# Kernel optimization log

Hardware: AMD Instinct MI355X
Metric: run time of the kernel (lower is better)

The kernel has to match this reference:

```python
import jax, jax.numpy as jnp
import numpy as np

NUM_HEADS = 16

def setup_inputs() -> dict:
    key = jax.random.key(0)
    k_x, k_wq, k_bq, k_wo, k_bo = jax.random.split(key, 5)
    B, S, D = 4, 2048, 1024
    x = jax.random.normal(k_x, (B, S, D), dtype=jnp.float32)
    # Flax Dense default init: lecun_normal for kernel, zeros for bias; use small normals here.
    w_qkv = jax.random.normal(k_wq, (D, 3 * D), dtype=jnp.float32) * (D ** -0.5)
    b_qkv = jnp.zeros((3 * D,), dtype=jnp.float32)
    w_out = jax.random.normal(k_wo, (D, D), dtype=jnp.float32) * (D ** -0.5)
    b_out = jnp.zeros((D,), dtype=jnp.float32)
    return {"x": x, "w_qkv": w_qkv, "b_qkv": b_qkv, "w_out": w_out, "b_out": b_out}

def reference(x, w_qkv, b_qkv, w_out, b_out):
    B, S, D = x.shape
    H = NUM_HEADS
    hd = D // H
    scale = hd ** -0.5
    qkv = x @ w_qkv + b_qkv                                  # [B,S,3D]
    qkv = qkv.reshape(B, S, 3, H, hd)
    qkv = jnp.transpose(qkv, (2, 0, 3, 1, 4))                # [3,B,H,S,hd]
    q, k, v = qkv[0], qkv[1], qkv[2]
    attn = jnp.einsum("bhqd,bhkd->bhqk", q, k) * scale       # [B,H,S,S]
    attn = jax.nn.softmax(attn, axis=-1)
    out = jnp.einsum("bhqk,bhkd->bhqd", attn, v)             # [B,H,S,hd]
    out = jnp.transpose(out, (0, 2, 1, 3)).reshape(B, S, D)
    return out @ w_out + b_out
```

## Files before the change

### kernel.cpp

```cpp
#include <hip/hip_runtime.h>
#include <cstdint>
#include <cstddef>

#define B_    4
#define S_    2048
#define D_    1024
#define H_    16
#define HD_   64
#define M_    8192
#define NQKV  3072

typedef __bf16 bf16;
typedef __bf16 bf16x4 __attribute__((ext_vector_type(4)));
typedef __bf16 bf16x8 __attribute__((ext_vector_type(8)));
typedef float  f32x2  __attribute__((ext_vector_type(2)));
typedef float  f32x4  __attribute__((ext_vector_type(4)));
typedef float  f32x16 __attribute__((ext_vector_type(16)));
typedef uint32_t u32x2 __attribute__((ext_vector_type(2)));
typedef uint32_t u32x4 __attribute__((ext_vector_type(4)));

#define MFMA16(a, b, c) __builtin_amdgcn_mfma_f32_16x16x32_bf16(a, b, c, 0, 0, 0)

__device__ __forceinline__ void gl2lds16(const void* g, void* l) {
  __builtin_amdgcn_global_load_lds(
      (__attribute__((address_space(1))) void*)(uintptr_t)g,
      (__attribute__((address_space(3))) void*)l, 16, 0, 0);
}

__device__ __forceinline__ uint32_t pkbf16(float a, float b) {
  union { bf16 h[2]; uint32_t u; } z;
  z.h[0] = (bf16)a; z.h[1] = (bf16)b;
  return z.u;
}

__global__ __launch_bounds__(256) void cast_f32_bf16(const float* __restrict__ in,
                                                     bf16* __restrict__ out, int n4) {
  int i = blockIdx.x * 256 + threadIdx.x;
  if (i >= n4) return;
  float4 v = ((const float4*)in)[i];
  bf16x4 o;
  o[0] = (bf16)v.x; o[1] = (bf16)v.y; o[2] = (bf16)v.z; o[3] = (bf16)v.w;
  ((bf16x4*)out)[i] = o;
}

__global__ __launch_bounds__(256) void transpose_cast(const float* __restrict__ in,
                                                      bf16* __restrict__ out, int R, int C) {
  __shared__ float tile[32][33];
  int bx = blockIdx.x * 32, by = blockIdx.y * 32;
  int tx = threadIdx.x, ty = threadIdx.y;
#pragma unroll
  for (int i = 0; i < 32; i += 8)
    tile[ty + i][tx] = in[(size_t)(by + ty + i) * C + bx + tx];
  __syncthreads();
#pragma unroll
  for (int i = 0; i < 32; i += 8)
    out[(size_t)(bx + ty + i) * R + by + tx] = (bf16)tile[tx][ty + i];
}

template <bool OUT_BF16>
__global__ __launch_bounds__(512, 2) void gemm256(const bf16* __restrict__ A,
                                                  const bf16* __restrict__ Bt,
                                                  const float* __restrict__ bias,
                                                  void* __restrict__ Cptr,
                                                  int M, int N, int K) {
  extern __shared__ __align__(16) bf16 sm[];
  const int tid  = threadIdx.x;
  const int lane = tid & 63, w = tid >> 6;
  const int lo   = lane & 15, quad = lane >> 4;
  const int wr   = w >> 1, wc = w & 1;
  const int xcd  = blockIdx.x & 7, g = blockIdx.x >> 3;
  const int mi_  = g & 3, n_ = g >> 2;
  const int bm   = (xcd * 4 + mi_) * 256, bn = n_ * 128;

  const bf16* Ag = A  + (size_t)bm * K;
  const bf16* Bg = Bt + (size_t)bn * K;

  const int swzl  = lo & 7;
  const int laneA = (wr * 64 + lo) * 64;
  const int laneB = (wc * 64 + lo) * 64;
  const int pc0   = (quad ^ swzl) * 8;
  const int pc1   = ((4 + quad) ^ swzl) * 8;

  int aoffG[4], boffG[2];
#pragma unroll
  for (int la = 0; la < 4; ++la) {
    int ca = la * 512 + tid, row = ca >> 3, s = ca & 7;
    aoffG[la] = row * K + ((s ^ (row & 7)) * 8);
  }
#pragma unroll
  for (int lb = 0; lb < 2; ++lb) {
    int cb = lb * 512 + tid, row = cb >> 3, s = cb & 7;
    boffG[lb] = row * K + ((s ^ (row & 7)) * 8);
  }
  const int T = K >> 6;

  f32x4 acc[4][4];
  const f32x4 zero = {0.f, 0.f, 0.f, 0.f};
#pragma unroll
  for (int i = 0; i < 4; ++i)
#pragma unroll
    for (int j = 0; j < 4; ++j) acc[i][j] = zero;

#pragma unroll
  for (int la = 0; la < 4; ++la)
    gl2lds16(Ag + aoffG[la], sm + (la * 512 + tid) * 8);
#pragma unroll
  for (int lb = 0; lb < 2; ++lb)
    gl2lds16(Bg + boffG[lb], sm + 16384 + (lb * 512 + tid) * 8);
#pragma unroll
  for (int la = 0; la < 4; ++la)
    gl2lds16(Ag + 64 + aoffG[la], sm + 24576 + (la * 512 + tid) * 8);
#pragma unroll
  for (int lb = 0; lb < 2; ++lb)
    gl2lds16(Bg + 64 + boffG[lb], sm + 24576 + 16384 + (lb * 512 + tid) * 8);
  asm volatile("s_waitcnt vmcnt(6)" ::: "memory");
  __builtin_amdgcn_s_barrier();

  auto body = [&](int t, bool st) __attribute__((always_inline)) {
    bf16* As_ = sm + (t % 3) * 24576;
    bf16* Bs_ = As_ + 16384;
    bf16* An_ = sm + ((t + 2) % 3) * 24576;
    bf16* Bn_ = An_ + 16384;
    const size_t kg = (size_t)(t + 2) * 64;
    bf16x8 av0, av1, bv[4];

    av0 = *(const bf16x8*)&As_[laneA + 0 * 1024 + pc0];
    av1 = *(const bf16x8*)&As_[laneA + 1 * 1024 + pc0];
#pragma unroll
    for (int j = 0; j < 4; ++j)
      bv[j] = *(const bf16x8*)&Bs_[laneB + j * 1024 + pc0];
    if (st) {
      gl2lds16(Ag + kg + aoffG[0], An_ + (0 * 512 + tid) * 8);
      gl2lds16(Ag + kg + aoffG[1], An_ + (1 * 512 + tid) * 8);
    }
    __builtin_amdgcn_s_barrier();
    __builtin_amdgcn_s_setprio(1);
#pragma unroll
    for (int j = 0; j < 4; ++j) {
      acc[0][j] = MFMA16(av0, bv[j], acc[0][j]);
      acc[1][j] = MFMA16(av1, bv[j], acc[1][j]);
    }
    __builtin_amdgcn_s_setprio(0);

    av0 = *(const bf16x8*)&As_[laneA + 2 * 1024 + pc0];
    av1 = *(const bf16x8*)&As_[laneA + 3 * 1024 + pc0];
    if (st) {
      gl2lds16(Ag + kg + aoffG[2], An_ + (2 * 512 + tid) * 8);
      gl2lds16(Ag + kg + aoffG[3], An_ + (3 * 512 + tid) * 8);
    }
    __builtin_amdgcn_s_barrier();
    __builtin_amdgcn_s_setprio(1);
#pragma unroll
    for (int j = 0; j < 4; ++j) {
      acc[2][j] = MFMA16(av0, bv[j], acc[2][j]);
      acc[3][j] = MFMA16(av1, bv[j], acc[3][j]);
    }
    __builtin_amdgcn_s_setprio(0);

    av0 = *(const bf16x8*)&As_[laneA + 0 * 1024 + pc1];
    av1 = *(const bf16x8*)&As_[laneA + 1 * 1024 + pc1];
#pragma unroll
    for (int j = 0; j < 4; ++j)
      bv[j] = *(const bf16x8*)&Bs_[laneB + j * 1024 + pc1];
    if (st)
      gl2lds16(Bg + kg + boffG[0], Bn_ + (0 * 512 + tid) * 8);
    __builtin_amdgcn_s_barrier();
    __builtin_amdgcn_s_setprio(1);
#pragma unroll
    for (int j = 0; j < 4; ++j) {
      acc[0][j] = MFMA16(av0, bv[j], acc[0][j]);
      acc[1][j] = MFMA16(av1, bv[j], acc[1][j]);
    }
    __builtin_amdgcn_s_setprio(0);

    av0 = *(const bf16x8*)&As_[laneA + 2 * 1024 + pc1];
    av1 = *(const bf16x8*)&As_[laneA + 3 * 1024 + pc1];
    if (st)
      gl2lds16(Bg + kg + boffG[1], Bn_ + (1 * 512 + tid) * 8);
    __builtin_amdgcn_s_barrier();
    __builtin_amdgcn_s_setprio(1);
#pragma unroll
    for (int j = 0; j < 4; ++j) {
      acc[2][j] = MFMA16(av0, bv[j], acc[2][j]);
      acc[3][j] = MFMA16(av1, bv[j], acc[3][j]);
    }
    __builtin_amdgcn_s_setprio(0);
  };

#pragma unroll 1
  for (int t = 0; t < T - 2; ++t) {
    body(t, true);
    asm volatile("s_waitcnt vmcnt(6)" ::: "memory");
    __builtin_amdgcn_s_barrier();
  }
  body(T - 2, false);
  asm volatile("s_waitcnt vmcnt(0)" ::: "memory");
  __builtin_amdgcn_s_barrier();
  body(T - 1, false);

#pragma unroll
  for (int j = 0; j < 4; ++j) {
    int cg = bn + wc * 64 + j * 16 + lo;
    float bsv = bias[cg];
#pragma unroll
    for (int i = 0; i < 4; ++i) {
      int rg = bm + wr * 64 + i * 16 + quad * 4;
#pragma unroll
      for (int r = 0; r < 4; ++r) {
        float v = acc[i][j][r] + bsv;
        if (OUT_BF16) ((bf16*)Cptr)[(size_t)(rg + r) * N + cg] = (bf16)v;
        else          ((float*)Cptr)[(size_t)(rg + r) * N + cg] = v;
      }
    }
  }
}

__global__ __launch_bounds__(256, 2) void flash_attn(const bf16* __restrict__ qkv,
                                                     bf16* __restrict__ out) {
  __shared__ __align__(16) bf16 smem[16384];
  bf16* const Ksm = smem;
  bf16* const Vsm = smem + 8192;

  const int tid  = threadIdx.x;
  const int lane = tid & 63, wq = tid >> 6;
  const int l31  = lane & 31;
  const int e    = lane >> 5;
  const int hi8  = e * 8, hi4 = e * 4;

  const int bid = blockIdx.x;
  const int qb  = bid >> 6;
  const int bh  = bid & 63;
  const int h   = bh & 15;
  const int b   = bh >> 4;
  const int q0  = qb * 256;
  const size_t rowb = (size_t)b * S_;
  const bf16* qbase = qkv + rowb * NQKV + h * HD_;
  const bf16* kbase = qbase + D_;
  const bf16* vbase = qbase + 2 * D_;

  bf16x8 qfA[4], qfB[4];
  {
    const bf16* qrow0 = qbase + (size_t)(q0 + wq * 64 + l31) * NQKV;
    const bf16* qrow1 = qrow0 + (size_t)32 * NQKV;
#pragma unroll
    for (int c = 0; c < 4; ++c) {
      qfA[c] = *(const bf16x8*)(qrow0 + c * 16 + hi8);
      qfB[c] = *(const bf16x8*)(qrow1 + c * 16 + hi8);
    }
  }

  int kq_off[2];
#pragma unroll
  for (int it = 0; it < 2; ++it) {
    int ci = it * 256 + tid;
    int s  = ci >> 3;
    int x  = (ci & 7) ^ (s & 7);
    kq_off[it] = s * NQKV + x * 8;
  }
  int vs_d[2], vs_s[2], vs_off[2];
#pragma unroll
  for (int u = 0; u < 2; ++u) {
    int idx = u * 256 + tid;
    int d0 = (idx & 31) * 2;
    int s0 = (idx >> 5) * 4;
    vs_d[u] = d0;
    vs_s[u] = s0;
    vs_off[u] = (((s0 >> 3) ^ ((d0 >> 1) & 7)) * 8) + (s0 & 7);
  }

  uint32_t vreg[2][4];

#pragma unroll
  for (int it = 0; it < 2; ++it)
    gl2lds16(kbase + kq_off[it], Ksm + (it * 256 + wq * 64) * 8);
#pragma unroll
  for (int u = 0; u < 2; ++u)
#pragma unroll
    for (int j = 0; j < 4; ++j)
      vreg[u][j] = *(const uint32_t*)(vbase + (size_t)(vs_s[u] + j) * NQKV + vs_d[u]);

  const f32x16 zero16 = {0.f,0.f,0.f,0.f,0.f,0.f,0.f,0.f,0.f,0.f,0.f,0.f,0.f,0.f,0.f,0.f};
  f32x16 oacc[2][2];
  oacc[0][0] = zero16; oacc[0][1] = zero16;
  oacc[1][0] = zero16; oacc[1][1] = zero16;
  f32x2 psA = {0.f, 0.f}, psB = {0.f, 0.f};
  const float c2 = 0.125f * 1.44269504088896341f;

  for (int kt = 0; kt < 32; ++kt) {
    const int buf = kt & 1;
#pragma unroll
    for (int u = 0; u < 2; ++u) {
      int d0 = vs_d[u];
      uint32_t lo0 = __builtin_amdgcn_perm(vreg[u][1], vreg[u][0], 0x05040100u);
      uint32_t lo1 = __builtin_amdgcn_perm(vreg[u][3], vreg[u][2], 0x05040100u);
      uint32_t hi0 = __builtin_amdgcn_perm(vreg[u][1], vreg[u][0], 0x07060302u);
      uint32_t hi1 = __builtin_amdgcn_perm(vreg[u][3], vreg[u][2], 0x07060302u);
      u32x2 lov = {lo0, lo1}, hiv = {hi0, hi1};
      *(u32x2*)&Vsm[buf * 4096 + (d0 + 0) * 64 + vs_off[u]] = lov;
      *(u32x2*)&Vsm[buf * 4096 + (d0 + 1) * 64 + vs_off[u]] = hiv;
    }
    __syncthreads();

    {
      int ktn = (kt + 1 < 32) ? kt + 1 : 31;
      const bf16* kb = kbase + (size_t)ktn * 64 * NQKV;
#pragma unroll
      for (int it = 0; it < 2; ++it)
        gl2lds16(kb + kq_off[it], Ksm + (buf ^ 1) * 4096 + (it * 256 + wq * 64) * 8);
    }
    {
      int ktn = (kt + 1 < 32) ? kt + 1 : 31;
      const bf16* vb = vbase + (size_t)ktn * 64 * NQKV;
#pragma unroll
      for (int u = 0; u < 2; ++u)
#pragma unroll
        for (int j = 0; j < 4; ++j)
          vreg[u][j] = *(const uint32_t*)(vb + (size_t)(vs_s[u] + j) * NQKV + vs_d[u]);
    }

#pragma unroll
    for (int kk = 0; kk < 2; ++kk) {
      f32x16 sA = zero16, sB = zero16;
      int srow = kk * 32 + l31;
      int swz  = (srow & 7) * 8;
      __builtin_amdgcn_s_setprio(1);
#pragma unroll
      for (int c = 0; c < 4; ++c) {
        bf16x8 kf = *(const bf16x8*)&Ksm[buf * 4096 + srow * 64 + ((c * 16 + hi8) ^ swz)];
        sA = __builtin_amdgcn_mfma_f32_32x32x16_bf16(kf, qfA[c], sA, 0, 0, 0);
        sB = __builtin_amdgcn_mfma_f32_32x32x16_bf16(kf, qfB[c], sB, 0, 0, 0);
      }
      __builtin_amdgcn_s_setprio(0);

      uint32_t Q8a[8], Q8b[8];
#pragma unroll
      for (int i = 0; i < 8; ++i) {
        f32x2 sva, svb;
        sva[0] = sA[2 * i]; sva[1] = sA[2 * i + 1];
        svb[0] = sB[2 * i]; svb[1] = sB[2 * i + 1];
        f32x2 ta = sva * c2 - 16.0f;
        f32x2 tb = svb * c2 - 16.0f;
        float a0 = __builtin_amdgcn_exp2f(ta[0]);
        float a1 = __builtin_amdgcn_exp2f(ta[1]);
        float b0 = __builtin_amdgcn_exp2f(tb[0]);
        float b1 = __builtin_amdgcn_exp2f(tb[1]);
        psA += (f32x2){a0, a1};
        psB += (f32x2){b0, b1};
        Q8a[i] = pkbf16(a0, a1);
        Q8b[i] = pkbf16(b0, b1);
      }

#pragma unroll
      for (int mh = 0; mh < 2; ++mh) {
        const int m = kk * 2 + mh, bq = mh * 4;
        u32x4 pda, pdb;
#if __has_builtin(__builtin_amdgcn_permlane32_swap)
        u32x2 wa0 = __builtin_amdgcn_permlane32_swap(Q8a[bq],     Q8a[bq + 2], false, false);
        u32x2 wa1 = __builtin_amdgcn_permlane32_swap(Q8a[bq + 1], Q8a[bq + 3], false, false);
        pda[0] = wa0[0]; pda[1] = wa1[0]; pda[2] = wa0[1]; pda[3] = wa1[1];
        u32x2 wb0 = __builtin_amdgcn_permlane32_swap(Q8b[bq],     Q8b[bq + 2], false, false);
        u32x2 wb1 = __builtin_amdgcn_permlane32_swap(Q8b[bq + 1], Q8b[bq + 3], false, false);
        pdb[0] = wb0[0]; pdb[1] = wb1[0]; pdb[2] = wb0[1]; pdb[3] = wb1[1];
#else
        {
          uint32_t s0 = e ? Q8a[bq]     : Q8a[bq + 2];
          uint32_t s1 = e ? Q8a[bq + 1] : Q8a[bq + 3];
          uint32_t r0 = __shfl_xor(s0, 32);
          uint32_t r1 = __shfl_xor(s1, 32);
          pda[0] = e ? r0 : Q8a[bq];
          pda[1] = e ? r1 : Q8a[bq + 1];
          pda[2] = e ? Q8a[bq + 2] : r0;
          pda[3] = e ? Q8a[bq + 3] : r1;
        }
        {
          uint32_t s0 = e ? Q8b[bq]     : Q8b[bq + 2];
          uint32_t s1 = e ? Q8b[bq + 1] : Q8b[bq + 3];
          uint32_t r0 = __shfl_xor(s0, 32);
          uint32_t r1 = __shfl_xor(s1, 32);
          pdb[0] = e ? r0 : Q8b[bq];
          pdb[1] = e ? r1 : Q8b[bq + 1];
          pdb[2] = e ? Q8b[bq + 2] : r0;
          pdb[3] = e ? Q8b[bq + 3] : r1;
        }
#endif
        bf16x8 pfa = __builtin_bit_cast(bf16x8, pda);
        bf16x8 pfb = __builtin_bit_cast(bf16x8, pdb);
        __builtin_amdgcn_s_setprio(1);
#pragma unroll
        for (int dt = 0; dt < 2; ++dt) {
          int drow = dt * 32 + l31;
          int swv  = (drow >> 1) & 7;
          bf16x8 vf = *(const bf16x8*)&Vsm[buf * 4096 + drow * 64 + (((m * 2 + e) ^ swv) * 8)];
          oacc[dt][0] = __builtin_amdgcn_mfma_f32_32x32x16_bf16(vf, pfa, oacc[dt][0], 0, 0, 0);
          oacc[dt][1] = __builtin_amdgcn_mfma_f32_32x32x16_bf16(vf, pfb, oacc[dt][1], 0, 0, 0);
        }
        __builtin_amdgcn_s_setprio(0);
      }
    }
  }

  float lsumA = psA[0] + psA[1];
  float lsumB = psB[0] + psB[1];
  lsumA += __shfl_xor(lsumA, 32);
  lsumB += __shfl_xor(lsumB, 32);

  __syncthreads();
  bf16* Os = smem;
  {
    float invA = 1.f / lsumA;
    float invB = 1.f / lsumB;
#pragma unroll
    for (int qs = 0; qs < 2; ++qs) {
      float inv = qs ? invB : invA;
      int ql = wq * 64 + qs * 32 + l31;
      int swO = (ql >> 1) & 7;
#pragma unroll
      for (int dt = 0; dt < 2; ++dt) {
#pragma unroll
        for (int g = 0; g < 4; ++g) {
          bf16x4 ov;
#pragma unroll
          for (int jj = 0; jj < 4; ++jj)
            ov[jj] = (bf16)(oacc[dt][qs][g * 4 + jj] * inv);
          *(bf16x4*)&Os[ql * 64 + (((dt * 4 + g) ^ swO) * 8) + hi4] = ov;
        }
      }
    }
  }
  __syncthreads();
#pragma unroll
  for (int it = 0; it < 8; ++it) {
    int idx = it * 256 + tid;
    int row = idx >> 3, c8 = idx & 7;
    bf16x8 t = *(const bf16x8*)&Os[row * 64 + ((c8 ^ ((row >> 1) & 7)) * 8)];
    *(bf16x8*)&out[(rowb + q0 + row) * D_ + h * HD_ + c8 * 8] = t;
  }
}

extern "C" void kernel_launch(void* const* d_in, const int* in_sizes, int n_in,
                              void* d_out, int out_size, void* d_ws, size_t ws_size,
                              hipStream_t stream) {
  const float* x     = (const float*)d_in[0];
  const float* w_qkv = (const float*)d_in[1];
  const float* b_qkv = (const float*)d_in[2];
  const float* w_out = (const float*)d_in[3];
  const float* b_out = (const float*)d_in[4];
  float* out = (float*)d_out;

  char* ws = (char*)d_ws;
  bf16* xb    = (bf16*)(ws);
  bf16* wqkvT = (bf16*)(ws + (size_t)16777216);
  bf16* woutT = (bf16*)(ws + (size_t)23068672);
  bf16* qkvb  = (bf16*)(ws + (size_t)25165824);
  bf16* attnb = (bf16*)(ws + (size_t)75497472);

  static int attr_done = 0;
  if (!attr_done) {
    hipFuncSetAttribute(reinterpret_cast<const void*>(&gemm256<true>),
                        hipFuncAttributeMaxDynamicSharedMemorySize, 147456);
    hipFuncSetAttribute(reinterpret_cast<const void*>(&gemm256<false>),
                        hipFuncAttributeMaxDynamicSharedMemorySize, 147456);
    attr_done = 1;
  }

  cast_f32_bf16<<<(M_ * D_ / 4 + 255) / 256, 256, 0, stream>>>(x, xb, M_ * D_ / 4);
  transpose_cast<<<dim3(NQKV / 32, D_ / 32), dim3(32, 8), 0, stream>>>(w_qkv, wqkvT, D_, NQKV);
  transpose_cast<<<dim3(D_ / 32, D_ / 32), dim3(32, 8), 0, stream>>>(w_out, woutT, D_, D_);

  gemm256<true><<<(M_ / 256) * (NQKV / 128), 512, 147456, stream>>>(
      xb, wqkvT, b_qkv, (void*)qkvb, M_, NQKV, D_);

  flash_attn<<<B_ * H_ * (S_ / 256), 256, 0, stream>>>(qkvb, attnb);

  gemm256<false><<<(M_ / 256) * (D_ / 128), 512, 147456, stream>>>(
      attnb, woutT, b_out, (void*)out, M_, D_, D_);
}
```

Before: 273.3 us.

## Add 256x256-tile ping-pong GEMM for QKV projection with interleaved prefetch

Adds a new GEMM kernel using 256x256 output tiles (8 waves in a 2x4 layout) with double-buffered LDS. Global-to-LDS prefetches for the next K tiles are interleaved with four MFMA phases that are separated by barriers and raised wave priority. The QKV projection now uses this kernel, which halves the grid and doubles per-block operand reuse. In exchange it needs more accumulator registers per wave, and the hand-tuned vmcnt waits must be exactly right for correctness.

```diff
diff --git a/kernel.cpp b/kernel.cpp
--- a/kernel.cpp
+++ b/kernel.cpp
@@ -55,6 +55,188 @@
 #pragma unroll
   for (int i = 0; i < 32; i += 8)
     out[(size_t)(bx + ty + i) * R + by + tx] = (bf16)tile[tx][ty + i];
+}
+
+template <bool OUT_BF16>
+__global__ __launch_bounds__(512, 2) void gemm8p(const bf16* __restrict__ A,
+                                                 const bf16* __restrict__ Bt,
+                                                 const float* __restrict__ bias,
+                                                 void* __restrict__ Cptr,
+                                                 int M, int N, int K) {
+  extern __shared__ __align__(16) bf16 sm8[];
+  const int tid  = threadIdx.x;
+  const int lane = tid & 63, w = tid >> 6;
+  const int lo   = lane & 15, quad = lane >> 4;
+  const int wr   = w >> 2, wc = w & 3;
+  const int xcd  = blockIdx.x & 7, g = blockIdx.x >> 3;
+  const int mi_  = g & 3, n_ = g >> 2;
+  const int bm   = (xcd * 4 + mi_) * 256, bn = n_ * 256;
+
+  const bf16* Ag = A  + (size_t)bm * K;
+  const bf16* Bg = Bt + (size_t)bn * K;
+
+  const int swz = lo & 7;
+  const int pc0 = (quad ^ swz) * 8;
+  const int pc1 = ((4 + quad) ^ swz) * 8;
+
+  int aoffG[4], boffG[4];
+#pragma unroll
+  for (int l = 0; l < 4; ++l) {
+    int c = l * 512 + tid, lam = c >> 3, s = c & 7;
+    aoffG[l] = lam * K + ((s ^ (lam & 7)) * 8);
+    int h = lam >> 7, q = (lam >> 5) & 3, sub = lam & 31;
+    boffG[l] = (q * 64 + h * 32 + sub) * K + ((s ^ (lam & 7)) * 8);
+  }
+
+  f32x4 acc[8][4];
+  const f32x4 zero = {0.f, 0.f, 0.f, 0.f};
+#pragma unroll
+  for (int i = 0; i < 8; ++i)
+#pragma unroll
+    for (int j = 0; j < 4; ++j) acc[i][j] = zero;
+
+  {
+    bf16* A0b = sm8;
+    bf16* B0b = sm8 + 16384;
+    bf16* A1b = sm8 + 32768;
+    bf16* B1b = sm8 + 49152;
+    gl2lds16(Ag + aoffG[0], A0b + (0 * 512 + tid) * 8);
+    gl2lds16(Ag + aoffG[1], A0b + (1 * 512 + tid) * 8);
+    gl2lds16(Bg + boffG[0], B0b + (0 * 512 + tid) * 8);
+    gl2lds16(Bg + boffG[1], B0b + (1 * 512 + tid) * 8);
+    gl2lds16(Ag + aoffG[2], A0b + (2 * 512 + tid) * 8);
+    gl2lds16(Ag + aoffG[3], A0b + (3 * 512 + tid) * 8);
+    gl2lds16(Bg + boffG[2], B0b + (2 * 512 + tid) * 8);
+    gl2lds16(Bg + boffG[3], B0b + (3 * 512 + tid) * 8);
+    gl2lds16(Ag + 64 + aoffG[0], A1b + (0 * 512 + tid) * 8);
+    gl2lds16(Ag + 64 + aoffG[1], A1b + (1 * 512 + tid) * 8);
+    gl2lds16(Bg + 64 + boffG[0], B1b + (0 * 512 + tid) * 8);
+    gl2lds16(Bg + 64 + boffG[1], B1b + (1 * 512 + tid) * 8);
+    gl2lds16(Ag + 64 + aoffG[2], A1b + (2 * 512 + tid) * 8);
+    gl2lds16(Ag + 64 + aoffG[3], A1b + (3 * 512 + tid) * 8);
+    asm volatile("s_waitcnt vmcnt(8)" ::: "memory");
+    __builtin_amdgcn_s_barrier();
+  }
+
+  auto do_tile = [&](int t, int mode) __attribute__((always_inline)) {
+    bf16* Ab = sm8 + (t & 1) * 32768;
+    bf16* Bb = Ab + 16384;
+    bf16* Ao = sm8 + ((t + 1) & 1) * 32768;
+    bf16* Bo = Ao + 16384;
+    const bf16* AgN = Ag + (size_t)(t + 2) * 64;
+    const bf16* BgN = Bg + (size_t)(t + 2) * 64;
+    const bf16* Bg1 = Bg + (size_t)(t + 1) * 64;
+
+    bf16x8 a03[8], a47[8], bfr[4];
+
+#pragma unroll
+    for (int mi = 0; mi < 4; ++mi) {
+      int rb = (wr * 128 + mi * 16 + lo) * 64;
+      a03[mi * 2 + 0] = *(const bf16x8*)&Ab[rb + pc0];
+      a03[mi * 2 + 1] = *(const bf16x8*)&Ab[rb + pc1];
+    }
+#pragma unroll
+    for (int nj = 0; nj < 2; ++nj) {
+      int rb = (wc * 32 + nj * 16 + lo) * 64;
+      bfr[nj * 2 + 0] = *(const bf16x8*)&Bb[rb + pc0];
+      bfr[nj * 2 + 1] = *(const bf16x8*)&Bb[rb + pc1];
+    }
+    if (mode >= 1) {
+      gl2lds16(Bg1 + boffG[2], Bo + (2 * 512 + tid) * 8);
+      gl2lds16(Bg1 + boffG[3], Bo + (3 * 512 + tid) * 8);
+    }
+    __builtin_amdgcn_s_setprio(1);
+#pragma unroll
+    for (int ks = 0; ks < 2; ++ks)
+#pragma unroll
+      for (int mi = 0; mi < 4; ++mi)
+#pragma unroll
+        for (int nj = 0; nj < 2; ++nj)
+          acc[mi][nj] = MFMA16(a03[mi * 2 + ks], bfr[nj * 2 + ks], acc[mi][nj]);
+    __builtin_amdgcn_s_setprio(0);
+    __builtin_amdgcn_s_barrier();
+
+#pragma unroll
+    for (int mi = 0; mi < 4; ++mi) {
+      int rb = (wr * 128 + (4 + mi) * 16 + lo) * 64;
+      a47[mi * 2 + 0] = *(const bf16x8*)&Ab[rb + pc0];
+      a47[mi * 2 + 1] = *(const bf16x8*)&Ab[rb + pc1];
+    }
+    __builtin_amdgcn_s_setprio(1);
+#pragma unroll
+    for (int ks = 0; ks < 2; ++ks)
+#pragma unroll
+      for (int mi = 0; mi < 4; ++mi)
+#pragma unroll
+        for (int nj = 0; nj < 2; ++nj)
+          acc[4 + mi][nj] = MFMA16(a47[mi * 2 + ks], bfr[nj * 2 + ks], acc[4 + mi][nj]);
+    __builtin_amdgcn_s_setprio(0);
+    if (mode == 0) { asm volatile("s_waitcnt vmcnt(0)" ::: "memory"); }
+    else           { asm volatile("s_waitcnt vmcnt(8)" ::: "memory"); }
+    __builtin_amdgcn_s_barrier();
+
+#pragma unroll
+    for (int nj = 0; nj < 2; ++nj) {
+      int rb = (128 + wc * 32 + nj * 16 + lo) * 64;
+      bfr[nj * 2 + 0] = *(const bf16x8*)&Bb[rb + pc0];
+      bfr[nj * 2 + 1] = *(const bf16x8*)&Bb[rb + pc1];
+    }
+    if (mode == 2) {
+      gl2lds16(AgN + aoffG[0], Ab + (0 * 512 + tid) * 8);
+      gl2lds16(AgN + aoffG[1], Ab + (1 * 512 + tid) * 8);
+      gl2lds16(BgN + boffG[0], Bb + (0 * 512 + tid) * 8);
+      gl2lds16(BgN + boffG[1], Bb + (1 * 512 + tid) * 8);
+    }
+    __builtin_amdgcn_s_setprio(1);
+#pragma unroll
+    for (int ks = 0; ks < 2; ++ks)
+#pragma unroll
+      for (int mi = 0; mi < 4; ++mi)
+#pragma unroll
+        for (int nj = 0; nj < 2; ++nj)
+          acc[4 + mi][2 + nj] = MFMA16(a47[mi * 2 + ks], bfr[nj * 2 + ks], acc[4 + mi][2 + nj]);
+    __builtin_amdgcn_s_setprio(0);
+    __builtin_amdgcn_s_barrier();
+
+    if (mode == 2) {
+      gl2lds16(AgN + aoffG[2], Ab + (2 * 512 + tid) * 8);
+      gl2lds16(AgN + aoffG[3], Ab + (3 * 512 + tid) * 8);
+    }
+    __builtin_amdgcn_s_setprio(1);
+#pragma unroll
+    for (int ks = 0; ks < 2; ++ks)
+#pragma unroll
+      for (int mi = 0; mi < 4; ++mi)
+#pragma unroll
+        for (int nj = 0; nj < 2; ++nj)
+          acc[mi][2 + nj] = MFMA16(a03[mi * 2 + ks], bfr[nj * 2 + ks], acc[mi][2 + nj]);
+    __builtin_amdgcn_s_setprio(0);
+    if (mode == 2)      { asm volatile("s_waitcnt vmcnt(8)" ::: "memory"); }
+    else if (mode == 1) { asm volatile("s_waitcnt vmcnt(2)" ::: "memory"); }
+    __builtin_amdgcn_s_barrier();
+  };
+
+  const int T = K >> 6;
+#pragma unroll 1
+  for (int t = 0; t < T - 2; ++t) do_tile(t, 2);
+  do_tile(T - 2, 1);
+  do_tile(T - 1, 0);
+
+#pragma unroll
+  for (int j = 0; j < 4; ++j) {
+    int cg = bn + wc * 64 + j * 16 + lo;
+    float bsv = bias[cg];
+#pragma unroll
+    for (int i = 0; i < 8; ++i) {
+      int rg = bm + wr * 128 + i * 16 + quad * 4;
+#pragma unroll
+      for (int r = 0; r < 4; ++r) {
+        float v = acc[i][j][r] + bsv;
+        if (OUT_BF16) ((bf16*)Cptr)[(size_t)(rg + r) * N + cg] = (bf16)v;
+        else          ((float*)Cptr)[(size_t)(rg + r) * N + cg] = v;
+      }
+    }
+  }
 }
 
 template <bool OUT_BF16>
@@ -456,8 +638,8 @@
 
   static int attr_done = 0;
   if (!attr_done) {
-    hipFuncSetAttribute(reinterpret_cast<const void*>(&gemm256<true>),
-                        hipFuncAttributeMaxDynamicSharedMemorySize, 147456);
+    hipFuncSetAttribute(reinterpret_cast<const void*>(&gemm8p<true>),
+                        hipFuncAttributeMaxDynamicSharedMemorySize, 131072);
     hipFuncSetAttribute(reinterpret_cast<const void*>(&gemm256<false>),
                         hipFuncAttributeMaxDynamicSharedMemorySize, 147456);
     attr_done = 1;
@@ -467,7 +649,7 @@
   transpose_cast<<<dim3(NQKV / 32, D_ / 32), dim3(32, 8), 0, stream>>>(w_qkv, wqkvT, D_, NQKV);
   transpose_cast<<<dim3(D_ / 32, D_ / 32), dim3(32, 8), 0, stream>>>(w_out, woutT, D_, D_);
 
-  gemm256<true><<<(M_ / 256) * (NQKV / 128), 512, 147456, stream>>>(
+  gemm8p<true><<<(M_ / 256) * (NQKV / 256), 512, 131072, stream>>>(
       xb, wqkvT, b_qkv, (void*)qkvb, M_, NQKV, D_);
 
   flash_attn<<<B_ * H_ * (S_ / 256), 256, 0, stream>>>(qkvb, attnb);
```

Result: slower. 279.4 us (+2.3%).

## Software-pipeline attention loop so QK^T of next tile overlaps softmax/PV

Applied to the files above, without the earlier changes.

Restructures the flash-attention key loop into a skewed pipeline: the QK^T MFMAs for tile kt+1 are issued right after the barrier, and the softmax and PV of tile kt run in the next iteration. K DMA and V register prefetch move earlier, to two tiles ahead for V. The goal is to overlap exp/pack VALU work with matrix work and hide load latency. The cost is more live accumulator registers (two S tiles held across iterations), which risks lower occupancy or spills.

```diff
diff --git a/kernel.cpp b/kernel.cpp
--- a/kernel.cpp
+++ b/kernel.cpp
@@ -270,74 +270,69 @@
 
   uint32_t vreg[2][4];
 
-#pragma unroll
-  for (int it = 0; it < 2; ++it)
-    gl2lds16(kbase + kq_off[it], Ksm + (it * 256 + wq * 64) * 8);
-#pragma unroll
-  for (int u = 0; u < 2; ++u)
-#pragma unroll
-    for (int j = 0; j < 4; ++j)
-      vreg[u][j] = *(const uint32_t*)(vbase + (size_t)(vs_s[u] + j) * NQKV + vs_d[u]);
-
   const f32x16 zero16 = {0.f,0.f,0.f,0.f,0.f,0.f,0.f,0.f,0.f,0.f,0.f,0.f,0.f,0.f,0.f,0.f};
   f32x16 oacc[2][2];
   oacc[0][0] = zero16; oacc[0][1] = zero16;
   oacc[1][0] = zero16; oacc[1][1] = zero16;
+  f32x16 sAc[2], sBc[2];
   f32x2 psA = {0.f, 0.f}, psB = {0.f, 0.f};
   const float c2 = 0.125f * 1.44269504088896341f;
 
-  for (int kt = 0; kt < 32; ++kt) {
-    const int buf = kt & 1;
-#pragma unroll
-    for (int u = 0; u < 2; ++u) {
-      int d0 = vs_d[u];
-      uint32_t lo0 = __builtin_amdgcn_perm(vreg[u][1], vreg[u][0], 0x05040100u);
-      uint32_t lo1 = __builtin_amdgcn_perm(vreg[u][3], vreg[u][2], 0x05040100u);
-      uint32_t hi0 = __builtin_amdgcn_perm(vreg[u][1], vreg[u][0], 0x07060302u);
-      uint32_t hi1 = __builtin_amdgcn_perm(vreg[u][3], vreg[u][2], 0x07060302u);
-      u32x2 lov = {lo0, lo1}, hiv = {hi0, hi1};
-      *(u32x2*)&Vsm[buf * 4096 + (d0 + 0) * 64 + vs_off[u]] = lov;
-      *(u32x2*)&Vsm[buf * 4096 + (d0 + 1) * 64 + vs_off[u]] = hiv;
-    }
-    __syncthreads();
-
-    {
-      int ktn = (kt + 1 < 32) ? kt + 1 : 31;
-      const bf16* kb = kbase + (size_t)ktn * 64 * NQKV;
-#pragma unroll
-      for (int it = 0; it < 2; ++it)
-        gl2lds16(kb + kq_off[it], Ksm + (buf ^ 1) * 4096 + (it * 256 + wq * 64) * 8);
-    }
-    {
-      int ktn = (kt + 1 < 32) ? kt + 1 : 31;
-      const bf16* vb = vbase + (size_t)ktn * 64 * NQKV;
-#pragma unroll
-      for (int u = 0; u < 2; ++u)
-#pragma unroll
-        for (int j = 0; j < 4; ++j)
-          vreg[u][j] = *(const uint32_t*)(vb + (size_t)(vs_s[u] + j) * NQKV + vs_d[u]);
-    }
-
+#define KDMA(KT, PB) {                                                      \
+    const bf16* kb_ = kbase + (size_t)(KT) * 64 * NQKV;                     \
+    _Pragma("unroll")                                                       \
+    for (int it = 0; it < 2; ++it)                                          \
+      gl2lds16(kb_ + kq_off[it], Ksm + (PB) * 4096 + (it * 256 + wq * 64) * 8); \
+  }
+#define VLOAD(KT) {                                                         \
+    const bf16* vb_ = vbase + (size_t)(KT) * 64 * NQKV;                     \
+    _Pragma("unroll")                                                       \
+    for (int u = 0; u < 2; ++u)                                             \
+      _Pragma("unroll")                                                     \
+      for (int j = 0; j < 4; ++j)                                           \
+        vreg[u][j] = *(const uint32_t*)(vb_ + (size_t)(vs_s[u] + j) * NQKV + vs_d[u]); \
+  }
+#define VWRITE(PB) {                                                        \
+    _Pragma("unroll")                                                       \
+    for (int u = 0; u < 2; ++u) {                                           \
+      int d0_ = vs_d[u];                                                    \
+      uint32_t lo0 = __builtin_amdgcn_perm(vreg[u][1], vreg[u][0], 0x05040100u); \
+      uint32_t lo1 = __builtin_amdgcn_perm(vreg[u][3], vreg[u][2], 0x05040100u); \
+      uint32_t hi0 = __builtin_amdgcn_perm(vreg[u][1], vreg[u][0], 0x07060302u); \
+      uint32_t hi1 = __builtin_amdgcn_perm(vreg[u][3], vreg[u][2], 0x07060302u); \
+      u32x2 lov = {lo0, lo1}, hiv = {hi0, hi1};                             \
+      *(u32x2*)&Vsm[(PB) * 4096 + (d0_ + 0) * 64 + vs_off[u]] = lov;        \
+      *(u32x2*)&Vsm[(PB) * 4096 + (d0_ + 1) * 64 + vs_off[u]] = hiv;        \
+    }                                                                       \
+  }
+
+  auto smfma = [&](int P) __attribute__((always_inline)) {
+    sAc[0] = zero16; sBc[0] = zero16;
+    sAc[1] = zero16; sBc[1] = zero16;
+    __builtin_amdgcn_s_setprio(1);
+#pragma unroll
+    for (int c = 0; c < 4; ++c) {
+#pragma unroll
+      for (int kk = 0; kk < 2; ++kk) {
+        int srow = kk * 32 + l31;
+        int swz  = (srow & 7) * 8;
+        bf16x8 kf = *(const bf16x8*)&Ksm[P * 4096 + srow * 64 + ((c * 16 + hi8) ^ swz)];
+        sAc[kk] = __builtin_amdgcn_mfma_f32_32x32x16_bf16(kf, qfA[c], sAc[kk], 0, 0, 0);
+        sBc[kk] = __builtin_amdgcn_mfma_f32_32x32x16_bf16(kf, qfB[c], sBc[kk], 0, 0, 0);
+      }
+    }
+    __builtin_amdgcn_s_setprio(0);
+  };
+
+  auto softpv = [&](int P) __attribute__((always_inline)) {
 #pragma unroll
     for (int kk = 0; kk < 2; ++kk) {
-      f32x16 sA = zero16, sB = zero16;
-      int srow = kk * 32 + l31;
-      int swz  = (srow & 7) * 8;
-      __builtin_amdgcn_s_setprio(1);
-#pragma unroll
-      for (int c = 0; c < 4; ++c) {
-        bf16x8 kf = *(const bf16x8*)&Ksm[buf * 4096 + srow * 64 + ((c * 16 + hi8) ^ swz)];
-        sA = __builtin_amdgcn_mfma_f32_32x32x16_bf16(kf, qfA[c], sA, 0, 0, 0);
-        sB = __builtin_amdgcn_mfma_f32_32x32x16_bf16(kf, qfB[c], sB, 0, 0, 0);
-      }
-      __builtin_amdgcn_s_setprio(0);
-
       uint32_t Q8a[8], Q8b[8];
 #pragma unroll
       for (int i = 0; i < 8; ++i) {
         f32x2 sva, svb;
-        sva[0] = sA[2 * i]; sva[1] = sA[2 * i + 1];
-        svb[0] = sB[2 * i]; svb[1] = sB[2 * i + 1];
+        sva[0] = sAc[kk][2 * i]; sva[1] = sAc[kk][2 * i + 1];
+        svb[0] = sBc[kk][2 * i]; svb[1] = sBc[kk][2 * i + 1];
         f32x2 ta = sva * c2 - 16.0f;
         f32x2 tb = svb * c2 - 16.0f;
         float a0 = __builtin_amdgcn_exp2f(ta[0]);
@@ -349,7 +344,6 @@
         Q8a[i] = pkbf16(a0, a1);
         Q8b[i] = pkbf16(b0, b1);
       }
-
 #pragma unroll
       for (int mh = 0; mh < 2; ++mh) {
         const int m = kk * 2 + mh, bq = mh * 4;
@@ -390,14 +384,40 @@
         for (int dt = 0; dt < 2; ++dt) {
           int drow = dt * 32 + l31;
           int swv  = (drow >> 1) & 7;
-          bf16x8 vf = *(const bf16x8*)&Vsm[buf * 4096 + drow * 64 + (((m * 2 + e) ^ swv) * 8)];
+          bf16x8 vf = *(const bf16x8*)&Vsm[P * 4096 + drow * 64 + (((m * 2 + e) ^ swv) * 8)];
           oacc[dt][0] = __builtin_amdgcn_mfma_f32_32x32x16_bf16(vf, pfa, oacc[dt][0], 0, 0, 0);
           oacc[dt][1] = __builtin_amdgcn_mfma_f32_32x32x16_bf16(vf, pfb, oacc[dt][1], 0, 0, 0);
         }
         __builtin_amdgcn_s_setprio(0);
       }
     }
-  }
+  };
+
+  KDMA(0, 0);
+  VLOAD(0);
+  VWRITE(0);
+  VLOAD(1);
+  __syncthreads();
+  smfma(0);
+
+#pragma unroll 1
+  for (int kt = 0; kt < 31; ++kt) {
+    const int buf = kt & 1;
+    KDMA(kt + 1, buf ^ 1);
+    VWRITE(buf ^ 1);
+    {
+      int kn2 = (kt + 2 < 32) ? kt + 2 : 31;
+      VLOAD(kn2);
+    }
+    softpv(buf);
+    __syncthreads();
+    smfma(buf ^ 1);
+  }
+  softpv(1);
+
+#undef KDMA
+#undef VLOAD
+#undef VWRITE
 
   float lsumA = psA[0] + psA[1];
   float lsumB = psB[0] + psB[1];
```

Result: no change. 277.1 us (+1.4%).
